# Kernel tuning notes

Hardware: AMD Instinct MI355X
Metric: run time of the kernel (lower is better)

The kernel has to match this reference:

```python
import jax, jax.numpy as jnp
import numpy as np

FORWARD_W = 1.0
BACKWARD_W = 1.0
NORMAL_W = 0.1
EPS = 1e-6


def setup_inputs() -> dict:
    key = jax.random.key(0)
    ks = jax.random.split(key, 5)
    N, M = 8192, 8192
    sp = jax.random.normal(ks[0], (N, 3), dtype=jnp.float32)
    tp = jax.random.normal(ks[1], (M, 3), dtype=jnp.float32)
    sn = jax.random.normal(ks[2], (N, 3), dtype=jnp.float32)
    tn = jax.random.normal(ks[3], (M, 3), dtype=jnp.float32)
    sn = sn / jnp.linalg.norm(sn, axis=1, keepdims=True)
    tn = tn / jnp.linalg.norm(tn, axis=1, keepdims=True)
    rot6d = jnp.array([1.0, 0.05, -0.02, 0.03, 1.0, 0.04], dtype=jnp.float32)
    rot6d = rot6d + 0.01 * jax.random.normal(ks[4], (6,), dtype=jnp.float32)
    return {
        'source_points': sp, 'target_points': tp,
        'source_normals': sn, 'target_normals': tn,
        'translation': jnp.zeros(3, jnp.float32),
        'rotation_6d': rot6d,
        'scale': jnp.ones(3, jnp.float32),
    }


def rotation_6d_to_matrix(r6):
    a1, a2 = r6[:3], r6[3:]
    b1 = a1 / jnp.linalg.norm(a1)
    b2 = a2 - jnp.sum(b1 * a2) * b1
    b2 = b2 / jnp.linalg.norm(b2)
    b3 = jnp.cross(b1, b2)
    return jnp.stack([b1, b2, b3], axis=1)  # (3,3), columns are b1,b2,b3


def cos_sim(a, b):
    na = jnp.maximum(jnp.linalg.norm(a, axis=1), EPS)
    nb = jnp.maximum(jnp.linalg.norm(b, axis=1), EPS)
    return jnp.sum(a * b, axis=1) / (na * nb)


def reference(source_points, target_points, source_normals, target_normals,
              translation, rotation_6d, scale):
    R = rotation_6d_to_matrix(rotation_6d)
    # apply_transformation: scale -> rotate -> translate
    src = (source_points * scale[None, :]) @ R.T + translation[None, :]  # (N,3)
    src_n = source_normals @ R.T  # (N,3)

    # pairwise squared distances (N,M)
    d2 = (jnp.sum(src * src, axis=1)[:, None]
          + jnp.sum(target_points * target_points, axis=1)[None, :]
          - 2.0 * src @ target_points.T)
    d2 = jnp.maximum(d2, 0.0)

    d_s2t = jnp.min(d2, axis=1)          # (N,) squared NN dist source->target
    idx_s = jnp.argmin(d2, axis=1)       # (N,)
    d_t2s = jnp.min(d2, axis=0)          # (M,)
    idx_t = jnp.argmin(d2, axis=0)       # (M,)

    loss = FORWARD_W * jnp.mean(d_s2t) + BACKWARD_W * jnp.mean(d_t2s)

    # normal loss: 1 - |cos| against matched normals (both directions)
    cn_s = 1.0 - jnp.abs(cos_sim(src_n, target_normals[idx_s]))
    cn_t = 1.0 - jnp.abs(cos_sim(target_normals, src_n[idx_t]))
    loss = loss + NORMAL_W * (jnp.mean(cn_s) + jnp.mean(cn_t))
    return loss
```

## Files before the change

kernel.cpp:

```cpp
#include <hip/hip_runtime.h>
#include <math.h>

#define FW 1.0f
#define BW 1.0f
#define NW 0.1f
#define EPSV 1e-6f

#define BT 256
#define MPT 4
#define JCH 256

__global__ __launch_bounds__(BT) void transform_kernel(
    const float* __restrict__ sp, const float* __restrict__ tp,
    const float* __restrict__ sn,
    const float* __restrict__ trans, const float* __restrict__ r6,
    const float* __restrict__ scl,
    float4* __restrict__ src4, float4* __restrict__ tgt4,
    float4* __restrict__ srcn4, float* __restrict__ out, int N, int M)
{
    int i = blockIdx.x * BT + threadIdx.x;

    if (blockIdx.y == 1) {
        if (i < M) {
            float x = tp[3*i], y = tp[3*i+1], z = tp[3*i+2];
            tgt4[i] = make_float4(x, y, z, x*x + y*y + z*z);
        }
        return;
    }

    if (i == 0) out[0] = 0.f;
    if (i >= N) return;

    float a1x = r6[0], a1y = r6[1], a1z = r6[2];
    float a2x = r6[3], a2y = r6[4], a2z = r6[5];
    float n1 = sqrtf(a1x*a1x + a1y*a1y + a1z*a1z);
    float b1x = a1x/n1, b1y = a1y/n1, b1z = a1z/n1;
    float dp = b1x*a2x + b1y*a2y + b1z*a2z;
    float u2x = a2x - dp*b1x, u2y = a2y - dp*b1y, u2z = a2z - dp*b1z;
    float n2 = sqrtf(u2x*u2x + u2y*u2y + u2z*u2z);
    float b2x = u2x/n2, b2y = u2y/n2, b2z = u2z/n2;
    float b3x = b1y*b2z - b1z*b2y;
    float b3y = b1z*b2x - b1x*b2z;
    float b3z = b1x*b2y - b1y*b2x;

    float qx = sp[3*i]   * scl[0];
    float qy = sp[3*i+1] * scl[1];
    float qz = sp[3*i+2] * scl[2];
    float sx = b1x*qx + b2x*qy + b3x*qz + trans[0];
    float sy = b1y*qx + b2y*qy + b3y*qz + trans[1];
    float sz = b1z*qx + b2z*qy + b3z*qz + trans[2];
    src4[i] = make_float4(sx, sy, sz, sx*sx + sy*sy + sz*sz);

    float nx = sn[3*i], ny = sn[3*i+1], nz = sn[3*i+2];
    float rx = b1x*nx + b2x*ny + b3x*nz;
    float ry = b1y*nx + b2y*ny + b3y*nz;
    float rz = b1z*nx + b2z*ny + b3z*nz;
    srcn4[i] = make_float4(rx, ry, rz, 0.f);
}

__global__ __launch_bounds__(BT) void min_kernel(
    const float4* __restrict__ src4, const float4* __restrict__ tgt4,
    unsigned long long* __restrict__ min_s,
    unsigned long long* __restrict__ min_t, int N, int M)
{
    const float4* A; const float4* B; unsigned long long* outm; int nA, nB;
    if (blockIdx.z == 0) { A = src4; B = tgt4; outm = min_s; nA = N; nB = M; }
    else                 { A = tgt4; B = src4; outm = min_t; nA = M; nB = N; }

    __shared__ float4 bs[JCH];
    const int tid   = threadIdx.x;
    const int aBase = blockIdx.x * (BT * MPT);
    const int jBase = blockIdx.y * JCH;

    float cx[MPT], cy[MPT], cz[MPT], s2[MPT], best[MPT];
    int bidx[MPT];
    #pragma unroll
    for (int p = 0; p < MPT; p++) {
        int ia = aBase + p*BT + tid;
        float4 a = A[ia < nA ? ia : 0];
        cx[p] = -2.f*a.x; cy[p] = -2.f*a.y; cz[p] = -2.f*a.z;
        s2[p] = a.w;
        best[p] = 3.4e38f; bidx[p] = 0;
    }
    {
        int jb = jBase + tid;
        bs[tid] = B[jb < nB ? jb : 0];
    }
    __syncthreads();

    const int jLim = (nB - jBase) < JCH ? (nB - jBase) : JCH;
    #pragma unroll 4
    for (int j = 0; j < jLim; j++) {
        float4 b = bs[j];
        #pragma unroll
        for (int p = 0; p < MPT; p++) {
            float d = fmaf(cx[p], b.x, b.w);
            d = fmaf(cy[p], b.y, d);
            d = fmaf(cz[p], b.z, d);
            d += s2[p];
            d = fmaxf(d, 0.f);
            if (d < best[p]) { best[p] = d; bidx[p] = jBase + j; }
        }
    }

    #pragma unroll
    for (int p = 0; p < MPT; p++) {
        int ia = aBase + p*BT + tid;
        if (ia < nA) {
            unsigned long long pk =
                ((unsigned long long)__float_as_uint(best[p]) << 32) |
                (unsigned int)bidx[p];
            atomicMin(&outm[ia], pk);
        }
    }
}

__global__ __launch_bounds__(BT) void reduce_kernel(
    const unsigned long long* __restrict__ min_s,
    const unsigned long long* __restrict__ min_t,
    const float4* __restrict__ srcn4, const float* __restrict__ tn,
    float* __restrict__ out, int N, int M)
{
    int gid = blockIdx.x * BT + threadIdx.x;
    float contrib = 0.f;

    if (gid < N) {
        unsigned long long pk = min_s[gid];
        float d = __uint_as_float((unsigned int)(pk >> 32));
        int idx = (int)(unsigned int)(pk & 0xffffffffull);
        float4 nv = srcn4[gid];
        float tx = tn[3*idx], ty = tn[3*idx+1], tz = tn[3*idx+2];
        float na = fmaxf(sqrtf(nv.x*nv.x + nv.y*nv.y + nv.z*nv.z), EPSV);
        float nb = fmaxf(sqrtf(tx*tx + ty*ty + tz*tz), EPSV);
        float cs = (nv.x*tx + nv.y*ty + nv.z*tz) / (na * nb);
        contrib = FW * d * (1.f/N) + NW * (1.f/N) * (1.f - fabsf(cs));
    } else if (gid < N + M) {
        int j = gid - N;
        unsigned long long pk = min_t[j];
        float d = __uint_as_float((unsigned int)(pk >> 32));
        int idx = (int)(unsigned int)(pk & 0xffffffffull);
        float tx = tn[3*j], ty = tn[3*j+1], tz = tn[3*j+2];
        float4 nv = srcn4[idx];
        float na = fmaxf(sqrtf(tx*tx + ty*ty + tz*tz), EPSV);
        float nb = fmaxf(sqrtf(nv.x*nv.x + nv.y*nv.y + nv.z*nv.z), EPSV);
        float cs = (tx*nv.x + ty*nv.y + tz*nv.z) / (na * nb);
        contrib = BW * d * (1.f/M) + NW * (1.f/M) * (1.f - fabsf(cs));
    }

    #pragma unroll
    for (int o = 32; o > 0; o >>= 1)
        contrib += __shfl_down(contrib, o, 64);

    __shared__ float wsum[BT/64];
    if ((threadIdx.x & 63) == 0) wsum[threadIdx.x >> 6] = contrib;
    __syncthreads();
    if (threadIdx.x == 0) {
        float s = 0.f;
        #pragma unroll
        for (int w = 0; w < BT/64; w++) s += wsum[w];
        atomicAdd(out, s);
    }
}

extern "C" void kernel_launch(void* const* d_in, const int* in_sizes, int n_in,
                              void* d_out, int out_size, void* d_ws, size_t ws_size,
                              hipStream_t stream) {
    const float* sp    = (const float*)d_in[0];
    const float* tp    = (const float*)d_in[1];
    const float* sn    = (const float*)d_in[2];
    const float* tn    = (const float*)d_in[3];
    const float* trans = (const float*)d_in[4];
    const float* r6    = (const float*)d_in[5];
    const float* scl   = (const float*)d_in[6];
    float* out = (float*)d_out;

    const int N = in_sizes[0] / 3;
    const int M = in_sizes[1] / 3;

    char* ws = (char*)d_ws;
    float4* src4  = (float4*)(ws);
    float4* tgt4  = (float4*)(ws + (size_t)16*N);
    float4* srcn4 = (float4*)(ws + (size_t)16*N + (size_t)16*M);
    unsigned long long* min_s =
        (unsigned long long*)(ws + (size_t)32*N + (size_t)16*M);
    unsigned long long* min_t = min_s + N;

    hipMemsetAsync(min_s, 0xFF, (size_t)(N + M) * 8, stream);

    int nmax = N > M ? N : M;
    dim3 tgrid((nmax + BT - 1) / BT, 2);
    transform_kernel<<<tgrid, BT, 0, stream>>>(sp, tp, sn, trans, r6, scl,
                                               src4, tgt4, srcn4, out, N, M);

    dim3 mgrid((N + BT*MPT - 1) / (BT*MPT), (M + JCH - 1) / JCH, 2);
    min_kernel<<<mgrid, BT, 0, stream>>>(src4, tgt4, min_s, min_t, N, M);

    int rblocks = (N + M + BT - 1) / BT;
    reduce_kernel<<<rblocks, BT, 0, stream>>>(min_s, min_t, srcn4, tn, out, N, M);
}
```

Baseline: 99.85 us.

## Fuse transform into min kernel and replace atomics with per-chunk partial minima

Drops the separate transform kernel and the memset. Each min-search block now transforms its own source and target points on the fly. The per-pair inner loop is cut down by deferring the |a|^2 add and the clamp until after the loop, and the argmin is written with selects. Atomic 64-bit mins are replaced by plain stores into a per-chunk partial buffer, which the finalize kernel min-reduces before computing the rotated normals. Tiles change to 8 points per thread and chunks of 128, which raises register pressure and makes the partial buffer larger (64 chunks × N × 8 bytes per direction).

```diff
diff --git a/kernel.cpp b/kernel.cpp
--- a/kernel.cpp
+++ b/kernel.cpp
@@ -6,145 +6,158 @@
 #define NW 0.1f
 #define EPSV 1e-6f
 
-#define BT 256
-#define MPT 4
-#define JCH 256
-
-__global__ __launch_bounds__(BT) void transform_kernel(
+#define BT  256
+#define MPT 8
+#define JCH 128
+
+#define COMPUTE_R(r6)                                                         \
+    float a1x = (r6)[0], a1y = (r6)[1], a1z = (r6)[2];                        \
+    float a2x = (r6)[3], a2y = (r6)[4], a2z = (r6)[5];                        \
+    float n1 = sqrtf(a1x*a1x + a1y*a1y + a1z*a1z);                            \
+    float b1x = a1x/n1, b1y = a1y/n1, b1z = a1z/n1;                           \
+    float dp = b1x*a2x + b1y*a2y + b1z*a2z;                                   \
+    float u2x = a2x - dp*b1x, u2y = a2y - dp*b1y, u2z = a2z - dp*b1z;         \
+    float n2 = sqrtf(u2x*u2x + u2y*u2y + u2z*u2z);                            \
+    float b2x = u2x/n2, b2y = u2y/n2, b2z = u2z/n2;                           \
+    float b3x = b1y*b2z - b1z*b2y;                                            \
+    float b3y = b1z*b2x - b1x*b2z;                                            \
+    float b3z = b1x*b2y - b1y*b2x;
+
+__global__ __launch_bounds__(BT) void chamfer_min(
     const float* __restrict__ sp, const float* __restrict__ tp,
-    const float* __restrict__ sn,
     const float* __restrict__ trans, const float* __restrict__ r6,
     const float* __restrict__ scl,
-    float4* __restrict__ src4, float4* __restrict__ tgt4,
-    float4* __restrict__ srcn4, float* __restrict__ out, int N, int M)
+    unsigned long long* __restrict__ part0,
+    unsigned long long* __restrict__ part1,
+    float* __restrict__ out, int N, int M)
 {
-    int i = blockIdx.x * BT + threadIdx.x;
-
-    if (blockIdx.y == 1) {
-        if (i < M) {
-            float x = tp[3*i], y = tp[3*i+1], z = tp[3*i+2];
-            tgt4[i] = make_float4(x, y, z, x*x + y*y + z*z);
-        }
-        return;
-    }
-
-    if (i == 0) out[0] = 0.f;
-    if (i >= N) return;
-
-    float a1x = r6[0], a1y = r6[1], a1z = r6[2];
-    float a2x = r6[3], a2y = r6[4], a2z = r6[5];
-    float n1 = sqrtf(a1x*a1x + a1y*a1y + a1z*a1z);
-    float b1x = a1x/n1, b1y = a1y/n1, b1z = a1z/n1;
-    float dp = b1x*a2x + b1y*a2y + b1z*a2z;
-    float u2x = a2x - dp*b1x, u2y = a2y - dp*b1y, u2z = a2z - dp*b1z;
-    float n2 = sqrtf(u2x*u2x + u2y*u2y + u2z*u2z);
-    float b2x = u2x/n2, b2y = u2y/n2, b2z = u2z/n2;
-    float b3x = b1y*b2z - b1z*b2y;
-    float b3y = b1z*b2x - b1x*b2z;
-    float b3z = b1x*b2y - b1y*b2x;
-
-    float qx = sp[3*i]   * scl[0];
-    float qy = sp[3*i+1] * scl[1];
-    float qz = sp[3*i+2] * scl[2];
-    float sx = b1x*qx + b2x*qy + b3x*qz + trans[0];
-    float sy = b1y*qx + b2y*qy + b3y*qz + trans[1];
-    float sz = b1z*qx + b2z*qy + b3z*qz + trans[2];
-    src4[i] = make_float4(sx, sy, sz, sx*sx + sy*sy + sz*sz);
-
-    float nx = sn[3*i], ny = sn[3*i+1], nz = sn[3*i+2];
-    float rx = b1x*nx + b2x*ny + b3x*nz;
-    float ry = b1y*nx + b2y*ny + b3y*nz;
-    float rz = b1z*nx + b2z*ny + b3z*nz;
-    srcn4[i] = make_float4(rx, ry, rz, 0.f);
-}
-
-__global__ __launch_bounds__(BT) void min_kernel(
-    const float4* __restrict__ src4, const float4* __restrict__ tgt4,
-    unsigned long long* __restrict__ min_s,
-    unsigned long long* __restrict__ min_t, int N, int M)
-{
-    const float4* A; const float4* B; unsigned long long* outm; int nA, nB;
-    if (blockIdx.z == 0) { A = src4; B = tgt4; outm = min_s; nA = N; nB = M; }
-    else                 { A = tgt4; B = src4; outm = min_t; nA = M; nB = N; }
+    const int tid  = threadIdx.x;
+    const int dir  = blockIdx.z;
+    const int nA   = dir ? M : N;
+    const int nB   = dir ? N : M;
+    const int jBase = blockIdx.y * JCH;
+    const int aBase = blockIdx.x * (BT * MPT);
+
+    if (dir == 0 && blockIdx.x == 0 && blockIdx.y == 0 && tid == 0)
+        out[0] = 0.f;
+
+    if (jBase >= nB || aBase >= nA) return;
+
+    COMPUTE_R(r6)
+    float t0 = trans[0], t1 = trans[1], t2v = trans[2];
+    float s0 = scl[0],  s1 = scl[1],  s2c = scl[2];
 
     __shared__ float4 bs[JCH];
-    const int tid   = threadIdx.x;
-    const int aBase = blockIdx.x * (BT * MPT);
-    const int jBase = blockIdx.y * JCH;
+    if (tid < JCH) {
+        int j = jBase + tid; if (j >= nB) j = nB - 1;
+        float x, y, z;
+        if (dir == 0) { x = tp[3*j]; y = tp[3*j+1]; z = tp[3*j+2]; }
+        else {
+            float qx = sp[3*j]*s0, qy = sp[3*j+1]*s1, qz = sp[3*j+2]*s2c;
+            x = b1x*qx + b2x*qy + b3x*qz + t0;
+            y = b1y*qx + b2y*qy + b3y*qz + t1;
+            z = b1z*qx + b2z*qy + b3z*qz + t2v;
+        }
+        bs[tid] = make_float4(x, y, z, x*x + y*y + z*z);
+    }
 
     float cx[MPT], cy[MPT], cz[MPT], s2[MPT], best[MPT];
-    int bidx[MPT];
+    int bj[MPT];
     #pragma unroll
     for (int p = 0; p < MPT; p++) {
-        int ia = aBase + p*BT + tid;
-        float4 a = A[ia < nA ? ia : 0];
-        cx[p] = -2.f*a.x; cy[p] = -2.f*a.y; cz[p] = -2.f*a.z;
-        s2[p] = a.w;
-        best[p] = 3.4e38f; bidx[p] = 0;
-    }
-    {
-        int jb = jBase + tid;
-        bs[tid] = B[jb < nB ? jb : 0];
+        int ia = aBase + p*BT + tid; if (ia >= nA) ia = 0;
+        float x, y, z;
+        if (dir == 0) {
+            float qx = sp[3*ia]*s0, qy = sp[3*ia+1]*s1, qz = sp[3*ia+2]*s2c;
+            x = b1x*qx + b2x*qy + b3x*qz + t0;
+            y = b1y*qx + b2y*qy + b3y*qz + t1;
+            z = b1z*qx + b2z*qy + b3z*qz + t2v;
+        } else { x = tp[3*ia]; y = tp[3*ia+1]; z = tp[3*ia+2]; }
+        cx[p] = -2.f*x; cy[p] = -2.f*y; cz[p] = -2.f*z;
+        s2[p] = x*x + y*y + z*z;
+        best[p] = 3.4e38f; bj[p] = 0;
     }
     __syncthreads();
 
-    const int jLim = (nB - jBase) < JCH ? (nB - jBase) : JCH;
+    int jLim = nB - jBase; if (jLim > JCH) jLim = JCH;
     #pragma unroll 4
     for (int j = 0; j < jLim; j++) {
         float4 b = bs[j];
         #pragma unroll
         for (int p = 0; p < MPT; p++) {
-            float d = fmaf(cx[p], b.x, b.w);
-            d = fmaf(cy[p], b.y, d);
-            d = fmaf(cz[p], b.z, d);
-            d += s2[p];
-            d = fmaxf(d, 0.f);
-            if (d < best[p]) { best[p] = d; bidx[p] = jBase + j; }
-        }
-    }
-
+            float e = fmaf(cz[p], b.z, b.w);
+            e = fmaf(cy[p], b.y, e);
+            e = fmaf(cx[p], b.x, e);
+            bool c = e < best[p];
+            best[p] = c ? e : best[p];
+            bj[p]   = c ? j : bj[p];
+        }
+    }
+
+    unsigned long long* pbase =
+        (dir == 0 ? part0 : part1) + (size_t)blockIdx.y * nA;
     #pragma unroll
     for (int p = 0; p < MPT; p++) {
         int ia = aBase + p*BT + tid;
         if (ia < nA) {
+            float d = fmaxf(best[p] + s2[p], 0.f);
             unsigned long long pk =
-                ((unsigned long long)__float_as_uint(best[p]) << 32) |
-                (unsigned int)bidx[p];
-            atomicMin(&outm[ia], pk);
+                ((unsigned long long)__float_as_uint(d) << 32) |
+                (unsigned int)(jBase + bj[p]);
+            pbase[ia] = pk;
         }
     }
 }
 
-__global__ __launch_bounds__(BT) void reduce_kernel(
-    const unsigned long long* __restrict__ min_s,
-    const unsigned long long* __restrict__ min_t,
-    const float4* __restrict__ srcn4, const float* __restrict__ tn,
-    float* __restrict__ out, int N, int M)
+__global__ __launch_bounds__(BT) void finalize(
+    const unsigned long long* __restrict__ part0,
+    const unsigned long long* __restrict__ part1,
+    const float* __restrict__ sn, const float* __restrict__ tn,
+    const float* __restrict__ r6,
+    float* __restrict__ out, int N, int M, int nChunkT, int nChunkS)
 {
-    int gid = blockIdx.x * BT + threadIdx.x;
+    const int gid = blockIdx.x * BT + threadIdx.x;
     float contrib = 0.f;
 
+    COMPUTE_R(r6)
+
     if (gid < N) {
-        unsigned long long pk = min_s[gid];
-        float d = __uint_as_float((unsigned int)(pk >> 32));
-        int idx = (int)(unsigned int)(pk & 0xffffffffull);
-        float4 nv = srcn4[gid];
+        const unsigned long long* b = part0 + gid;
+        unsigned long long m = ~0ull;
+        for (int c = 0; c < nChunkT; c++) {
+            unsigned long long v = b[(size_t)c * N];
+            m = v < m ? v : m;
+        }
+        float d = __uint_as_float((unsigned int)(m >> 32));
+        int idx = (int)(unsigned int)(m & 0xffffffffull);
+        float nx = sn[3*gid], ny = sn[3*gid+1], nz = sn[3*gid+2];
+        float rx = b1x*nx + b2x*ny + b3x*nz;
+        float ry = b1y*nx + b2y*ny + b3y*nz;
+        float rz = b1z*nx + b2z*ny + b3z*nz;
         float tx = tn[3*idx], ty = tn[3*idx+1], tz = tn[3*idx+2];
-        float na = fmaxf(sqrtf(nv.x*nv.x + nv.y*nv.y + nv.z*nv.z), EPSV);
+        float na = fmaxf(sqrtf(rx*rx + ry*ry + rz*rz), EPSV);
         float nb = fmaxf(sqrtf(tx*tx + ty*ty + tz*tz), EPSV);
-        float cs = (nv.x*tx + nv.y*ty + nv.z*tz) / (na * nb);
-        contrib = FW * d * (1.f/N) + NW * (1.f/N) * (1.f - fabsf(cs));
+        float cs = (rx*tx + ry*ty + rz*tz) / (na * nb);
+        contrib = (FW * d + NW * (1.f - fabsf(cs))) * (1.f / N);
     } else if (gid < N + M) {
         int j = gid - N;
-        unsigned long long pk = min_t[j];
-        float d = __uint_as_float((unsigned int)(pk >> 32));
-        int idx = (int)(unsigned int)(pk & 0xffffffffull);
+        const unsigned long long* b = part1 + j;
+        unsigned long long m = ~0ull;
+        for (int c = 0; c < nChunkS; c++) {
+            unsigned long long v = b[(size_t)c * M];
+            m = v < m ? v : m;
+        }
+        float d = __uint_as_float((unsigned int)(m >> 32));
+        int idx = (int)(unsigned int)(m & 0xffffffffull);
         float tx = tn[3*j], ty = tn[3*j+1], tz = tn[3*j+2];
-        float4 nv = srcn4[idx];
+        float nx = sn[3*idx], ny = sn[3*idx+1], nz = sn[3*idx+2];
+        float rx = b1x*nx + b2x*ny + b3x*nz;
+        float ry = b1y*nx + b2y*ny + b3y*nz;
+        float rz = b1z*nx + b2z*ny + b3z*nz;
         float na = fmaxf(sqrtf(tx*tx + ty*ty + tz*tz), EPSV);
-        float nb = fmaxf(sqrtf(nv.x*nv.x + nv.y*nv.y + nv.z*nv.z), EPSV);
-        float cs = (tx*nv.x + ty*nv.y + tz*nv.z) / (na * nb);
-        contrib = BW * d * (1.f/M) + NW * (1.f/M) * (1.f - fabsf(cs));
+        float nb = fmaxf(sqrtf(rx*rx + ry*ry + rz*rz), EPSV);
+        float cs = (tx*rx + ty*ry + tz*rz) / (na * nb);
+        contrib = (BW * d + NW * (1.f - fabsf(cs))) * (1.f / M);
     }
 
     #pragma unroll
@@ -177,24 +190,19 @@
     const int N = in_sizes[0] / 3;
     const int M = in_sizes[1] / 3;
 
-    char* ws = (char*)d_ws;
-    float4* src4  = (float4*)(ws);
-    float4* tgt4  = (float4*)(ws + (size_t)16*N);
-    float4* srcn4 = (float4*)(ws + (size_t)16*N + (size_t)16*M);
-    unsigned long long* min_s =
-        (unsigned long long*)(ws + (size_t)32*N + (size_t)16*M);
-    unsigned long long* min_t = min_s + N;
-
-    hipMemsetAsync(min_s, 0xFF, (size_t)(N + M) * 8, stream);
-
-    int nmax = N > M ? N : M;
-    dim3 tgrid((nmax + BT - 1) / BT, 2);
-    transform_kernel<<<tgrid, BT, 0, stream>>>(sp, tp, sn, trans, r6, scl,
-                                               src4, tgt4, srcn4, out, N, M);
-
-    dim3 mgrid((N + BT*MPT - 1) / (BT*MPT), (M + JCH - 1) / JCH, 2);
-    min_kernel<<<mgrid, BT, 0, stream>>>(src4, tgt4, min_s, min_t, N, M);
+    const int nChunkT = (M + JCH - 1) / JCH;
+    const int nChunkS = (N + JCH - 1) / JCH;
+
+    unsigned long long* part0 = (unsigned long long*)d_ws;
+    unsigned long long* part1 = part0 + (size_t)nChunkT * N;
+
+    const int nmax = N > M ? N : M;
+    const int cmax = nChunkT > nChunkS ? nChunkT : nChunkS;
+    dim3 mgrid((nmax + BT*MPT - 1) / (BT*MPT), cmax, 2);
+    chamfer_min<<<mgrid, BT, 0, stream>>>(sp, tp, trans, r6, scl,
+                                          part0, part1, out, N, M);
 
     int rblocks = (N + M + BT - 1) / BT;
-    reduce_kernel<<<rblocks, BT, 0, stream>>>(min_s, min_t, srcn4, tn, out, N, M);
+    finalize<<<rblocks, BT, 0, stream>>>(part0, part1, sn, tn, r6,
+                                         out, N, M, nChunkT, nChunkS);
 }
```

New measurement: 109.3 us. 1.09x slower.
